# Optimization experiments

Measured on AMD Instinct MI355X. Metric: run time of the kernel, lower is better.

Reference implementation:

```python
import jax, jax.numpy as jnp
import numpy as np
from jax import lax

STRIDE = 1
PAD = 1


def setup_inputs() -> dict:
    key = jax.random.key(0)
    ks = jax.random.split(key, 6)
    B, C, H, W = 32, 256, 56, 56
    E, O, K = 4, 256, 3
    HID = max(C // 4, 8)  # 64
    return {
        "x": jax.random.normal(ks[0], (B, C, H, W), dtype=jnp.float32),
        "experts": jax.random.normal(ks[1], (E, O, C, K, K), dtype=jnp.float32),
        "rw1": jax.random.normal(ks[2], (HID, C), dtype=jnp.float32) * 0.05,
        "rb1": jax.random.normal(ks[3], (HID,), dtype=jnp.float32) * 0.05,
        "rw2": jax.random.normal(ks[4], (E, HID), dtype=jnp.float32) * 0.05,
        "rb2": jax.random.normal(ks[5], (E,), dtype=jnp.float32) * 0.05,
    }


def reference(x, experts, rw1, rb1, rw2, rb2):
    B, C, H, W = x.shape
    E, O, _, K, _ = experts.shape
    # Routing: global avg pool -> 1x1 conv (matmul) -> relu -> 1x1 conv -> softmax
    pooled = x.mean(axis=(2, 3))                      # [B, C]
    h = jax.nn.relu(pooled @ rw1.T + rb1)             # [B, HID]
    routing = jax.nn.softmax(h @ rw2.T + rb2, axis=-1)  # [B, E]
    # Per-sample mixed conv weights: [B, O, C, K, K]
    combined = jnp.einsum('be,eocij->bocij', routing, experts)
    # Per-sample conv as a single grouped conv: groups = B
    x_g = x.reshape(1, B * C, H, W)
    w_g = combined.reshape(B * O, C, K, K)
    out = lax.conv_general_dilated(
        x_g, w_g,
        window_strides=(STRIDE, STRIDE),
        padding=[(PAD, PAD), (PAD, PAD)],
        dimension_numbers=('NCHW', 'OIHW', 'NCHW'),
        feature_group_count=B,
    )  # [1, B*O, H', W']
    Ho, Wo = out.shape[2], out.shape[3]
    return out.reshape(B, O, Ho, Wo)
```

## Files before the change

### kernel.cpp

```cpp
#include <hip/hip_runtime.h>


#define B_  32
#define C_  256
#define H_  56
#define W_  56
#define HW_ 3136
#define E_  4
#define O_  256
#define HID_ 64
#define HP_ 58
#define PHW_ 3364
#define KK_ 2304

typedef __attribute__((ext_vector_type(8))) short bf16x8;
typedef __attribute__((ext_vector_type(4))) float f32x4;

__device__ __forceinline__ unsigned short f2bf(float f) {
    unsigned int u = __float_as_uint(f);
    u = (u + 0x7FFFu + ((u >> 16) & 1u)) >> 16;
    return (unsigned short)u;
}

__device__ __forceinline__ unsigned int cvt_pk_bf16(float lo, float hi) {
    unsigned int r;
    asm("v_cvt_pk_bf16_f32 %0, %1, %2" : "=v"(r) : "v"(lo), "v"(hi));
    return r;
}

__device__ __forceinline__ void load_lds16(const void* g, void* l) {
    __builtin_amdgcn_global_load_lds(
        (__attribute__((address_space(1))) unsigned int*)(unsigned long long)(const char*)g,
        (__attribute__((address_space(3))) unsigned int*)l,
        16, 0, 0);
}

__global__ __launch_bounds__(256) void transform_pool(const float* __restrict__ x,
                                                      unsigned short* __restrict__ xp,
                                                      float* __restrict__ pp) {
    const int h    = blockIdx.x;
    const int half = blockIdx.y;
    const int b    = blockIdx.z;
    const int t    = threadIdx.x;
    const int c0   = half * 128;
    __shared__ alignas(16) float tile[128 * 64];
    __shared__ alignas(16) float part[14 * 128];

    const float* src = x + ((size_t)(b * C_ + c0) * H_ + h) * W_;
#pragma unroll
    for (int i = t; i < 128 * 14; i += 256) {
        const int c  = i / 14;
        const int w4 = (i % 14) * 4;
        float4 v = *(const float4*)(src + (size_t)c * (H_ * W_) + w4);
        const int wsw = w4 ^ (((c >> 3) & 7) << 2);
        *(float4*)&tile[c * 64 + wsw] = v;
    }

    unsigned int* ubase = (unsigned int*)(xp + (size_t)b * PHW_ * C_);
    {
        const int hp = h + 1;
        if (t < 128) {
            const int col = (t >> 6) ? 57 : 0;
            const int cu  = t & 63;
            ubase[((size_t)hp * HP_ + col) * 128 + half * 64 + cu] = 0u;
        }
        if (h == 0) {
            for (int i = t; i < HP_ * 64; i += 256) {
                const int pix = i >> 6, cu = i & 63;
                ubase[(size_t)pix * 128 + half * 64 + cu] = 0u;
                ubase[((size_t)57 * HP_ + pix) * 128 + half * 64 + cu] = 0u;
            }
        }
    }
    __syncthreads();

    const int cu  = t & 15;
    const int seg = t >> 4;
    float s0 = 0.f, s1 = 0.f, s2 = 0.f, s3 = 0.f;
    float s4 = 0.f, s5 = 0.f, s6 = 0.f, s7 = 0.f;
    if (seg < 14) {
        const int sw = (cu & 7) << 2;
        unsigned short* ob = xp
            + ((size_t)(b * HP_ + h + 1) * HP_ + (seg * 4 + 1)) * C_ + c0 + cu * 8;
#pragma unroll
        for (int wi = 0; wi < 4; ++wi) {
            const int wc = (seg * 4 + wi) ^ sw;
            const float* tp = tile + cu * 512 + wc;
            float f0 = tp[0 * 64], f1 = tp[1 * 64], f2 = tp[2 * 64], f3 = tp[3 * 64];
            float f4 = tp[4 * 64], f5 = tp[5 * 64], f6 = tp[6 * 64], f7 = tp[7 * 64];
            s0 += f0; s1 += f1; s2 += f2; s3 += f3;
            s4 += f4; s5 += f5; s6 += f6; s7 += f7;
            uint4 pk;
            pk.x = cvt_pk_bf16(f0, f1);
            pk.y = cvt_pk_bf16(f2, f3);
            pk.z = cvt_pk_bf16(f4, f5);
            pk.w = cvt_pk_bf16(f6, f7);
            *(uint4*)(ob + (size_t)wi * C_) = pk;
        }
        *(float4*)&part[seg * 128 + cu * 8 + 0] = make_float4(s0, s1, s2, s3);
        *(float4*)&part[seg * 128 + cu * 8 + 4] = make_float4(s4, s5, s6, s7);
    }
    __syncthreads();
    if (t < 128) {
        float v = 0.f;
#pragma unroll
        for (int sgi = 0; sgi < 14; ++sgi) v += part[sgi * 128 + t];
        pp[((size_t)(b * C_ + c0 + t)) * 56 + h] = v;
    }
}

__global__ void routing_kernel(const float* __restrict__ pp,
                               const float* __restrict__ rw1,
                               const float* __restrict__ rb1,
                               const float* __restrict__ rw2,
                               const float* __restrict__ rb2,
                               float* __restrict__ routing) {
    const int b = blockIdx.x;
    const int t = threadIdx.x;
    __shared__ float pl[C_];
    __shared__ float part[256];
    __shared__ float hb[HID_];
    __shared__ float lg[E_];
    {
        const float* p = pp + (size_t)(b * C_ + t) * 56;
        float s = 0.f;
#pragma unroll
        for (int i = 0; i < 14; ++i) {
            float4 v = *(const float4*)(p + 4 * i);
            s += v.x + v.y + v.z + v.w;
        }
        pl[t] = s * (1.0f / (float)HW_);
    }
    __syncthreads();
    const int j = t >> 2, seg = t & 3;
    {
        const float* w = rw1 + j * C_ + seg * 64;
        const float* p = pl + seg * 64;
        float s = 0.0f;
#pragma unroll 8
        for (int cc = 0; cc < 64; ++cc) s += p[cc] * w[cc];
        part[t] = s;
    }
    __syncthreads();
    if (seg == 0) {
        float s = part[t] + part[t + 1] + part[t + 2] + part[t + 3] + rb1[j];
        hb[j] = fmaxf(s, 0.0f);
    }
    __syncthreads();
    if (t < E_) {
        float s = rb2[t];
        for (int jj = 0; jj < HID_; ++jj) s += hb[jj] * rw2[t * HID_ + jj];
        lg[t] = s;
    }
    __syncthreads();
    if (t == 0) {
        float mx = fmaxf(fmaxf(lg[0], lg[1]), fmaxf(lg[2], lg[3]));
        float e0 = expf(lg[0] - mx), e1 = expf(lg[1] - mx);
        float e2 = expf(lg[2] - mx), e3 = expf(lg[3] - mx);
        float inv = 1.0f / (e0 + e1 + e2 + e3);
        routing[b * E_ + 0] = e0 * inv;
        routing[b * E_ + 1] = e1 * inv;
        routing[b * E_ + 2] = e2 * inv;
        routing[b * E_ + 3] = e3 * inv;
    }
}

__global__ void combine_kernel(const float* __restrict__ experts,
                               const float* __restrict__ routing,
                               unsigned short* __restrict__ wcomb) {
    const int o  = blockIdx.x;
    const int bg = blockIdx.y;
    const int c  = threadIdx.x;
    __shared__ alignas(16) unsigned short sh[KK_];
    __shared__ float rt[16];
    if (c < 16) rt[c] = routing[bg * 16 + c];

    float w[E_][9];
#pragma unroll
    for (int e = 0; e < E_; ++e) {
        const float* ep = experts + ((size_t)(e * O_ + o) * C_ + c) * 9;
        float4 v0 = *(const float4*)(ep + 0);
        float4 v1 = *(const float4*)(ep + 4);
        w[e][0] = v0.x; w[e][1] = v0.y; w[e][2] = v0.z; w[e][3] = v0.w;
        w[e][4] = v1.x; w[e][5] = v1.y; w[e][6] = v1.z; w[e][7] = v1.w;
        w[e][8] = ep[8];
    }
    __syncthreads();
#pragma unroll
    for (int bq = 0; bq < 4; ++bq) {
        const float r0 = rt[bq * 4 + 0], r1 = rt[bq * 4 + 1];
        const float r2 = rt[bq * 4 + 2], r3 = rt[bq * 4 + 3];
#pragma unroll
        for (int k = 0; k < 9; ++k) {
            float a = r0 * w[0][k] + r1 * w[1][k] + r2 * w[2][k] + r3 * w[3][k];
            sh[k * C_ + c] = f2bf(a);
        }
        __syncthreads();
        const int b = bg * 4 + bq;
        uint4* dst = (uint4*)(wcomb + (size_t)(b * O_ + o) * KK_);
        const uint4* s4 = (const uint4*)sh;
        for (int idx = c; idx < KK_ / 8; idx += 256) dst[idx] = s4[idx];
        __syncthreads();
    }
}

__global__ __launch_bounds__(256, 4) void conv_gemm(const unsigned short* __restrict__ xp,
                                                    const unsigned short* __restrict__ wcomb,
                                                    float* __restrict__ out) {
    __shared__ alignas(16) unsigned short Alds[128 * 64];
    __shared__ alignas(16) unsigned short Blds[128 * 64];

    const int tid  = threadIdx.x;
    const int lane = tid & 63;
    const int wid  = tid >> 6;

    const int id = blockIdx.x;
    const int b  = (id >> 3) / 50 * 8 + (id & 7);
    const int t  = (id >> 3) % 50;
    const int o0 = (t & 1) * 128;
    const int n0 = (t >> 1) * 128;

    const int qg = (lane & 7) ^ ((lane >> 3) & 7);

    const unsigned short* aptr = wcomb
        + (size_t)(b * O_ + o0 + wid * 32 + (lane >> 3)) * KK_ + qg * 8;
    const unsigned short* bptr = xp + (size_t)b * PHW_ * C_ + qg * 8;
    unsigned int boff[4];
#pragma unroll
    for (int iss = 0; iss < 4; ++iss) {
        int p = n0 + wid * 32 + iss * 8 + (lane >> 3);
        if (p > HW_ - 1) p = HW_ - 1;
        boff[iss] = (unsigned int)((p / W_) * HP_ + (p % W_)) * C_;
    }
    unsigned short* aldst = (unsigned short*)Alds + (wid * 32) * 64;
    unsigned short* bldst = (unsigned short*)Blds + (wid * 32) * 64;

    f32x4 acc[4][4];
#pragma unroll
    for (int i = 0; i < 4; ++i)
#pragma unroll
        for (int j = 0; j < 4; ++j) acc[i][j] = (f32x4){0.f, 0.f, 0.f, 0.f};

    const int fm = lane & 15;
    const int fq = lane >> 4;
    const int wm = wid >> 1, wn = wid & 1;
    const int colk0 = ((0 + fq) ^ (fm & 7)) * 8;
    const int colk1 = ((4 + fq) ^ (fm & 7)) * 8;
    const unsigned short* ardb = (const unsigned short*)Alds + (wm * 64 + fm) * 64;
    const unsigned short* brdb = (const unsigned short*)Blds + (wn * 64 + fm) * 64;

    for (int kc = 0; kc < 36; ++kc) {
        const int r   = kc >> 2;
        const int duA = kc * 64;
        const int duB = ((r / 3) * HP_ + (r % 3)) * C_ + (kc & 3) * 64;
        __syncthreads();
#pragma unroll
        for (int iss = 0; iss < 4; ++iss) {
            load_lds16(aptr + (size_t)iss * (8 * KK_) + duA, aldst + iss * (8 * 64));
            load_lds16(bptr + boff[iss] + duB,              bldst + iss * (8 * 64));
        }
        __syncthreads();
#pragma unroll
        for (int ks = 0; ks < 2; ++ks) {
            const int col = ks ? colk1 : colk0;
            bf16x8 af[4], bv[4];
#pragma unroll
            for (int mi = 0; mi < 4; ++mi) af[mi] = *(const bf16x8*)(ardb + mi * (16 * 64) + col);
#pragma unroll
            for (int ni = 0; ni < 4; ++ni) bv[ni] = *(const bf16x8*)(brdb + ni * (16 * 64) + col);
#pragma unroll
            for (int mi = 0; mi < 4; ++mi)
#pragma unroll
                for (int ni = 0; ni < 4; ++ni)
                    acc[mi][ni] = __builtin_amdgcn_mfma_f32_16x16x32_bf16(
                        af[mi], bv[ni], acc[mi][ni], 0, 0, 0);
        }
    }

#pragma unroll
    for (int ni = 0; ni < 4; ++ni) {
        const int n = n0 + wn * 64 + ni * 16 + fm;
        if (n >= HW_) continue;
#pragma unroll
        for (int mi = 0; mi < 4; ++mi) {
            const int m = o0 + wm * 64 + mi * 16 + fq * 4;
            float* po = out + (size_t)(b * O_ + m) * HW_ + n;
#pragma unroll
            for (int rg = 0; rg < 4; ++rg) po[(size_t)rg * HW_] = acc[mi][ni][rg];
        }
    }
}

extern "C" void kernel_launch(void* const* d_in, const int* in_sizes, int n_in,
                              void* d_out, int out_size, void* d_ws, size_t ws_size,
                              hipStream_t stream) {
    const float* x       = (const float*)d_in[0];
    const float* experts = (const float*)d_in[1];
    const float* rw1     = (const float*)d_in[2];
    const float* rb1     = (const float*)d_in[3];
    const float* rw2     = (const float*)d_in[4];
    const float* rb2     = (const float*)d_in[5];
    float* out = (float*)d_out;

    const size_t XP_OFF = 0;
    const size_t WC_OFF = 55115776;
    const size_t PP_OFF = WC_OFF + 37748736;
    const size_t RT_OFF = PP_OFF + 1835008;
    unsigned short* xp    = (unsigned short*)((char*)d_ws + XP_OFF);
    unsigned short* wcomb = (unsigned short*)((char*)d_ws + WC_OFF);
    float* pp      = (float*)((char*)d_ws + PP_OFF);
    float* routing = (float*)((char*)d_ws + RT_OFF);

    transform_pool<<<dim3(H_, 2, B_), dim3(256), 0, stream>>>(x, xp, pp);
    routing_kernel<<<dim3(B_), dim3(256), 0, stream>>>(pp, rw1, rb1, rw2, rb2, routing);
    combine_kernel<<<dim3(O_, 8), dim3(256), 0, stream>>>(experts, routing, wcomb);
    conv_gemm<<<dim3(1600), dim3(256), 0, stream>>>(xp, wcomb, out);
}
```

Before: 329.3 us.

## Rewrite conv GEMM with 256x256 tiles, 8 waves and double-buffered async LDS pipeline

The implicit-GEMM conv kernel now uses 512-thread blocks, each computing a 256-output by 256-pixel tile, where before it used 256 threads on a 128x128 tile. Global-to-LDS loads are double buffered and interleaved with MFMA phases, using manual vmcnt waits, raw s_barrier and setprio, so loads overlap compute instead of sitting between full syncthreads. The larger tile reduces redundant A/B traffic per FLOP but cuts the grid to 416 blocks and raises register and LDS use (128KB LDS), which may limit occupancy and leave some CUs unevenly loaded.

```diff
diff --git a/kernel.cpp b/kernel.cpp
--- a/kernel.cpp
+++ b/kernel.cpp
@@ -34,6 +34,14 @@
         (__attribute__((address_space(3))) unsigned int*)l,
         16, 0, 0);
 }
+
+__device__ __forceinline__ void wgbar() {
+    asm volatile("" ::: "memory");
+    __builtin_amdgcn_s_barrier();
+    asm volatile("" ::: "memory");
+}
+
+#define VMW(N) asm volatile("s_waitcnt vmcnt(" #N ")" ::: "memory")
 
 __global__ __launch_bounds__(256) void transform_pool(const float* __restrict__ x,
                                                       unsigned short* __restrict__ xp,
@@ -204,91 +212,142 @@
     }
 }
 
-__global__ __launch_bounds__(256, 4) void conv_gemm(const unsigned short* __restrict__ xp,
-                                                    const unsigned short* __restrict__ wcomb,
-                                                    float* __restrict__ out) {
-    __shared__ alignas(16) unsigned short Alds[128 * 64];
-    __shared__ alignas(16) unsigned short Blds[128 * 64];
+__global__ __launch_bounds__(512) void conv_gemm(const unsigned short* __restrict__ xp,
+                                                 const unsigned short* __restrict__ wcomb,
+                                                 float* __restrict__ out) {
+    __shared__ alignas(16) unsigned short Alds[2 * 2 * 128 * 64];
+    __shared__ alignas(16) unsigned short Blds[2 * 2 * 128 * 64];
 
     const int tid  = threadIdx.x;
     const int lane = tid & 63;
     const int wid  = tid >> 6;
-
-    const int id = blockIdx.x;
-    const int b  = (id >> 3) / 50 * 8 + (id & 7);
-    const int t  = (id >> 3) % 50;
-    const int o0 = (t & 1) * 128;
-    const int n0 = (t >> 1) * 128;
-
+    const int wm   = wid >> 2;
+    const int wn   = wid & 3;
+    const int fm   = lane & 15;
+    const int fq   = lane >> 4;
+
+    const int id  = blockIdx.x;
+    const int xcd = id & 7;
+    const int qq  = id >> 3;
+    const int b   = (qq / 13) * 8 + xcd;
+    const int n0  = (qq % 13) * 256;
+
+    const int rl = wid * 8 + (lane >> 3);
     const int qg = (lane & 7) ^ ((lane >> 3) & 7);
-
-    const unsigned short* aptr = wcomb
-        + (size_t)(b * O_ + o0 + wid * 32 + (lane >> 3)) * KK_ + qg * 8;
-    const unsigned short* bptr = xp + (size_t)b * PHW_ * C_ + qg * 8;
-    unsigned int boff[4];
-#pragma unroll
-    for (int iss = 0; iss < 4; ++iss) {
-        int p = n0 + wid * 32 + iss * 8 + (lane >> 3);
-        if (p > HW_ - 1) p = HW_ - 1;
-        boff[iss] = (unsigned int)((p / W_) * HP_ + (p % W_)) * C_;
-    }
-    unsigned short* aldst = (unsigned short*)Alds + (wid * 32) * 64;
-    unsigned short* bldst = (unsigned short*)Blds + (wid * 32) * 64;
-
-    f32x4 acc[4][4];
-#pragma unroll
-    for (int i = 0; i < 4; ++i)
+    const unsigned short* abase = wcomb + ((size_t)b * O_ + rl) * KK_ + qg * 8;
+    const unsigned short* bbase = xp + (size_t)b * PHW_ * C_ + qg * 8;
+    unsigned int boffs[2][2];
+#pragma unroll
+    for (int u = 0; u < 2; ++u)
+#pragma unroll
+        for (int s = 0; s < 2; ++s) {
+            int pi = (u * 2 + (rl >> 5)) * 64 + s * 32 + (rl & 31);
+            int p  = n0 + pi;
+            if (p > HW_ - 1) p = HW_ - 1;
+            boffs[u][s] = (unsigned int)((p / W_) * HP_ + (p % W_)) * C_;
+        }
+
+#define STAGE_A(BUF, S, KT)                                                     \
+    {                                                                           \
+        const unsigned short* asrc_ = abase + (size_t)((S) * 64) * KK_ + (KT) * 64; \
+        load_lds16(asrc_,                    Alds + (((BUF) * 2 + (S)) * 128 + wid * 8) * 64);      \
+        load_lds16(asrc_ + (size_t)128 * KK_, Alds + (((BUF) * 2 + (S)) * 128 + 64 + wid * 8) * 64); \
+    }
+
+#define STAGE_B(BUF, S, KT)                                                     \
+    {                                                                           \
+        const int r9_  = (KT) >> 2;                                             \
+        const int duB_ = ((r9_ / 3) * HP_ + (r9_ % 3)) * C_ + ((KT) & 3) * 64;  \
+        load_lds16(bbase + boffs[0][S] + duB_, Blds + (((BUF) * 2 + (S)) * 128 + wid * 8) * 64);      \
+        load_lds16(bbase + boffs[1][S] + duB_, Blds + (((BUF) * 2 + (S)) * 128 + 64 + wid * 8) * 64); \
+    }
+
+    f32x4 acc[8][4];
+#pragma unroll
+    for (int i = 0; i < 8; ++i)
 #pragma unroll
         for (int j = 0; j < 4; ++j) acc[i][j] = (f32x4){0.f, 0.f, 0.f, 0.f};
-
-    const int fm = lane & 15;
-    const int fq = lane >> 4;
-    const int wm = wid >> 1, wn = wid & 1;
+    bf16x8 af[4][2];
+
     const int colk0 = ((0 + fq) ^ (fm & 7)) * 8;
     const int colk1 = ((4 + fq) ^ (fm & 7)) * 8;
-    const unsigned short* ardb = (const unsigned short*)Alds + (wm * 64 + fm) * 64;
-    const unsigned short* brdb = (const unsigned short*)Blds + (wn * 64 + fm) * 64;
-
-    for (int kc = 0; kc < 36; ++kc) {
-        const int r   = kc >> 2;
-        const int duA = kc * 64;
-        const int duB = ((r / 3) * HP_ + (r % 3)) * C_ + (kc & 3) * 64;
-        __syncthreads();
-#pragma unroll
-        for (int iss = 0; iss < 4; ++iss) {
-            load_lds16(aptr + (size_t)iss * (8 * KK_) + duA, aldst + iss * (8 * 64));
-            load_lds16(bptr + boff[iss] + duB,              bldst + iss * (8 * 64));
-        }
-        __syncthreads();
-#pragma unroll
-        for (int ks = 0; ks < 2; ++ks) {
-            const int col = ks ? colk1 : colk0;
-            bf16x8 af[4], bv[4];
-#pragma unroll
-            for (int mi = 0; mi < 4; ++mi) af[mi] = *(const bf16x8*)(ardb + mi * (16 * 64) + col);
-#pragma unroll
-            for (int ni = 0; ni < 4; ++ni) bv[ni] = *(const bf16x8*)(brdb + ni * (16 * 64) + col);
-#pragma unroll
-            for (int mi = 0; mi < 4; ++mi)
-#pragma unroll
-                for (int ni = 0; ni < 4; ++ni)
-                    acc[mi][ni] = __builtin_amdgcn_mfma_f32_16x16x32_bf16(
-                        af[mi], bv[ni], acc[mi][ni], 0, 0, 0);
-        }
-    }
-
-#pragma unroll
-    for (int ni = 0; ni < 4; ++ni) {
-        const int n = n0 + wn * 64 + ni * 16 + fm;
-        if (n >= HW_) continue;
-#pragma unroll
-        for (int mi = 0; mi < 4; ++mi) {
-            const int m = o0 + wm * 64 + mi * 16 + fq * 4;
-            float* po = out + (size_t)(b * O_ + m) * HW_ + n;
-#pragma unroll
-            for (int rg = 0; rg < 4; ++rg) po[(size_t)rg * HW_] = acc[mi][ni][rg];
-        }
-    }
+    const int arow  = (wm * 64 + fm) * 64;
+    const int brow  = (wn * 32 + fm) * 64;
+
+#define PHASE(MH, NH, BUF, WCODE, STAGE_STMT, RDAF)                             \
+    {                                                                           \
+        WCODE;                                                                  \
+        wgbar();                                                                \
+        if (RDAF) {                                                             \
+            _Pragma("unroll")                                                   \
+            for (int q_ = 0; q_ < 4; ++q_) {                                    \
+                af[q_][0] = *(const bf16x8*)(Alds + (((BUF) * 2 + (MH)) * 128) * 64 + arow + q_ * 1024 + colk0); \
+                af[q_][1] = *(const bf16x8*)(Alds + (((BUF) * 2 + (MH)) * 128) * 64 + arow + q_ * 1024 + colk1); \
+            }                                                                   \
+        }                                                                       \
+        bf16x8 bv[2][2];                                                        \
+        _Pragma("unroll")                                                       \
+        for (int j_ = 0; j_ < 2; ++j_) {                                        \
+            bv[j_][0] = *(const bf16x8*)(Blds + (((BUF) * 2 + (NH)) * 128) * 64 + brow + j_ * 1024 + colk0); \
+            bv[j_][1] = *(const bf16x8*)(Blds + (((BUF) * 2 + (NH)) * 128) * 64 + brow + j_ * 1024 + colk1); \
+        }                                                                       \
+        STAGE_STMT;                                                             \
+        asm volatile("" ::: "memory");                                          \
+        __builtin_amdgcn_s_setprio(1);                                          \
+        _Pragma("unroll")                                                       \
+        for (int q_ = 0; q_ < 4; ++q_)                                          \
+            _Pragma("unroll")                                                   \
+            for (int j_ = 0; j_ < 2; ++j_) {                                    \
+                acc[(MH) * 4 + q_][(NH) * 2 + j_] = __builtin_amdgcn_mfma_f32_16x16x32_bf16( \
+                    af[q_][0], bv[j_][0], acc[(MH) * 4 + q_][(NH) * 2 + j_], 0, 0, 0);       \
+                acc[(MH) * 4 + q_][(NH) * 2 + j_] = __builtin_amdgcn_mfma_f32_16x16x32_bf16( \
+                    af[q_][1], bv[j_][1], acc[(MH) * 4 + q_][(NH) * 2 + j_], 0, 0, 0);       \
+            }                                                                   \
+        __builtin_amdgcn_s_setprio(0);                                          \
+    }
+
+    STAGE_A(0, 0, 0); STAGE_B(0, 0, 0); STAGE_A(0, 1, 0); STAGE_B(0, 1, 0);
+    STAGE_A(1, 0, 1); STAGE_B(1, 0, 1);
+
+#pragma unroll 1
+    for (int i = 0; i < 17; ++i) {
+        const int k2 = 2 * i;
+        PHASE(0, 0, 0, VMW(8),  STAGE_A(1, 1, k2 + 1), 1)
+        PHASE(0, 1, 0, VMW(6),  STAGE_B(1, 1, k2 + 1), 0)
+        PHASE(1, 0, 0, VMW(10), STAGE_A(0, 0, k2 + 2), 1)
+        PHASE(1, 1, 0,        , STAGE_B(0, 0, k2 + 2), 0)
+        PHASE(0, 0, 1, VMW(8),  STAGE_A(0, 1, k2 + 2), 1)
+        PHASE(0, 1, 1, VMW(6),  STAGE_B(0, 1, k2 + 2), 0)
+        PHASE(1, 0, 1, VMW(10), STAGE_A(1, 0, k2 + 3), 1)
+        PHASE(1, 1, 1,        , STAGE_B(1, 0, k2 + 3), 0)
+    }
+    PHASE(0, 0, 0, VMW(8),  STAGE_A(1, 1, 35), 1)
+    PHASE(0, 1, 0, VMW(6),  STAGE_B(1, 1, 35), 0)
+    PHASE(1, 0, 0, VMW(10), (void)0, 1)
+    PHASE(1, 1, 0,        , (void)0, 0)
+    PHASE(0, 0, 1, VMW(4),  (void)0, 1)
+    PHASE(0, 1, 1, VMW(0),  (void)0, 0)
+    PHASE(1, 0, 1, VMW(0),  (void)0, 1)
+    PHASE(1, 1, 1,        , (void)0, 0)
+
+#pragma unroll
+    for (int mi = 0; mi < 8; ++mi) {
+        const int o = wm * 128 + mi * 16 + fq * 4;
+#pragma unroll
+        for (int ni = 0; ni < 4; ++ni) {
+            const int p = n0 + wn * 64 + ni * 16 + fm;
+            if (p < HW_) {
+                float* po = out + ((size_t)(b * O_ + o)) * HW_ + p;
+                po[0 * HW_] = acc[mi][ni][0];
+                po[1 * HW_] = acc[mi][ni][1];
+                po[2 * (size_t)HW_] = acc[mi][ni][2];
+                po[3 * (size_t)HW_] = acc[mi][ni][3];
+            }
+        }
+    }
+#undef PHASE
+#undef STAGE_A
+#undef STAGE_B
 }
 
 extern "C" void kernel_launch(void* const* d_in, const int* in_sizes, int n_in,
@@ -314,5 +373,5 @@
     transform_pool<<<dim3(H_, 2, B_), dim3(256), 0, stream>>>(x, xp, pp);
     routing_kernel<<<dim3(B_), dim3(256), 0, stream>>>(pp, rw1, rb1, rw2, rb2, routing);
     combine_kernel<<<dim3(O_, 8), dim3(256), 0, stream>>>(experts, routing, wcomb);
-    conv_gemm<<<dim3(1600), dim3(256), 0, stream>>>(xp, wcomb, out);
-}
+    conv_gemm<<<dim3(416), dim3(512), 0, stream>>>(xp, wcomb, out);
+}
```

Result: slower. 346.6 us (+5.2%).

## Double-buffer LDS tiles in conv GEMM to overlap loads with MFMA

Applied to the files above, without the earlier changes.

The conv GEMM main loop now uses two LDS buffers for the A and B tiles. It issues the global-to-LDS loads for the next K chunk before running the MFMAs on the current chunk, which cuts the barrier count per iteration from two to one. The goal is to hide global load latency behind compute. In exchange, LDS per block doubles to 64KB and the occupancy hint of 4 is dropped from launch bounds, which likely lowers resident blocks per CU.

```diff
diff --git a/kernel.cpp b/kernel.cpp
--- a/kernel.cpp
+++ b/kernel.cpp
@@ -204,11 +204,11 @@
     }
 }
 
-__global__ __launch_bounds__(256, 4) void conv_gemm(const unsigned short* __restrict__ xp,
-                                                    const unsigned short* __restrict__ wcomb,
-                                                    float* __restrict__ out) {
-    __shared__ alignas(16) unsigned short Alds[128 * 64];
-    __shared__ alignas(16) unsigned short Blds[128 * 64];
+__global__ __launch_bounds__(256) void conv_gemm(const unsigned short* __restrict__ xp,
+                                                 const unsigned short* __restrict__ wcomb,
+                                                 float* __restrict__ out) {
+    __shared__ alignas(16) unsigned short Alds[2][128 * 64];
+    __shared__ alignas(16) unsigned short Blds[2][128 * 64];
 
     const int tid  = threadIdx.x;
     const int lane = tid & 63;
@@ -232,8 +232,21 @@
         if (p > HW_ - 1) p = HW_ - 1;
         boff[iss] = (unsigned int)((p / W_) * HP_ + (p % W_)) * C_;
     }
-    unsigned short* aldst = (unsigned short*)Alds + (wid * 32) * 64;
-    unsigned short* bldst = (unsigned short*)Blds + (wid * 32) * 64;
+    const int ldo = (wid * 32) * 64;
+
+#define STAGE(BUF, KC)                                                          \
+    {                                                                           \
+        const int r_   = (KC) >> 2;                                             \
+        const int duA_ = (KC) * 64;                                             \
+        const int duB_ = ((r_ / 3) * HP_ + (r_ % 3)) * C_ + ((KC) & 3) * 64;    \
+        _Pragma("unroll")                                                       \
+        for (int iss_ = 0; iss_ < 4; ++iss_) {                                  \
+            load_lds16(aptr + (size_t)iss_ * (8 * KK_) + duA_,                  \
+                       &Alds[BUF][ldo + iss_ * (8 * 64)]);                      \
+            load_lds16(bptr + boff[iss_] + duB_,                                \
+                       &Blds[BUF][ldo + iss_ * (8 * 64)]);                      \
+        }                                                                       \
+    }
 
     f32x4 acc[4][4];
 #pragma unroll
@@ -246,20 +259,18 @@
     const int wm = wid >> 1, wn = wid & 1;
     const int colk0 = ((0 + fq) ^ (fm & 7)) * 8;
     const int colk1 = ((4 + fq) ^ (fm & 7)) * 8;
-    const unsigned short* ardb = (const unsigned short*)Alds + (wm * 64 + fm) * 64;
-    const unsigned short* brdb = (const unsigned short*)Blds + (wn * 64 + fm) * 64;
-
+    const int aro = (wm * 64 + fm) * 64;
+    const int bro = (wn * 64 + fm) * 64;
+
+    STAGE(0, 0)
+    __syncthreads();
+
+#pragma unroll 2
     for (int kc = 0; kc < 36; ++kc) {
-        const int r   = kc >> 2;
-        const int duA = kc * 64;
-        const int duB = ((r / 3) * HP_ + (r % 3)) * C_ + (kc & 3) * 64;
-        __syncthreads();
-#pragma unroll
-        for (int iss = 0; iss < 4; ++iss) {
-            load_lds16(aptr + (size_t)iss * (8 * KK_) + duA, aldst + iss * (8 * 64));
-            load_lds16(bptr + boff[iss] + duB,              bldst + iss * (8 * 64));
-        }
-        __syncthreads();
+        const int cur = kc & 1;
+        if (kc < 35) STAGE(cur ^ 1, kc + 1)
+        const unsigned short* ardb = &Alds[cur][aro];
+        const unsigned short* brdb = &Blds[cur][bro];
 #pragma unroll
         for (int ks = 0; ks < 2; ++ks) {
             const int col = ks ? colk1 : colk0;
@@ -275,7 +286,9 @@
                     acc[mi][ni] = __builtin_amdgcn_mfma_f32_16x16x32_bf16(
                         af[mi], bv[ni], acc[mi][ni], 0, 0, 0);
         }
-    }
+        __syncthreads();
+    }
+#undef STAGE
 
 #pragma unroll
     for (int ni = 0; ni < 4; ++ni) {
```

Result: slower. 367.7 us (+11.7%).
